# Kernel optimization log

Measured on AMD Instinct MI355X. Metric: run time of the kernel, lower is better.

## Reference

```python
import jax, jax.numpy as jnp
import numpy as np

# static config (matches init_kwargs)
B, H, W, C = 8, 64, 64, 512
HEADS, WS, SHIFT = 16, 8, 4
N = WS * WS
HIDDEN = 4 * C
HEAD_DIM = C // HEADS
SCALE = HEAD_DIM ** -0.5
EPS = 1e-3  # keras LayerNormalization default epsilon


def _rel_pos_index(ws):
    # replicates tf.meshgrid default 'xy' indexing used in the source
    coords = np.stack(np.meshgrid(np.arange(ws), np.arange(ws)))  # [2, ws, ws]
    cf = coords.reshape(2, -1)
    rel = (cf[:, :, None] - cf[:, None, :]).transpose(1, 2, 0)  # [N, N, 2]
    rel[:, :, 0] += ws - 1
    rel[:, :, 1] += ws - 1
    rel[:, :, 0] *= 2 * ws - 1
    return jnp.asarray(rel.sum(-1))  # [N, N] int


def _attn_mask(h, w, ws, shift):
    img = np.zeros((h, w), dtype=np.float32)
    cnt = 0
    for hs in (slice(0, -ws), slice(-ws, -shift), slice(-shift, None)):
        for wsl in (slice(0, -ws), slice(-ws, -shift), slice(-shift, None)):
            img[hs, wsl] = cnt
            cnt += 1
    mw = img.reshape(h // ws, ws, w // ws, ws).transpose(0, 2, 1, 3).reshape(-1, ws * ws)  # [nW, N]
    diff = mw[:, None, :] - mw[:, :, None]
    return jnp.asarray(np.where(diff != 0, -100.0, 0.0).astype(np.float32))  # [nW, N, N]


REL_IDX = _rel_pos_index(WS)
ATTN_MASK = _attn_mask(H, W, WS, SHIFT)
NW = (H // WS) * (W // WS)


def _ln(x, g, b):
    mu = jnp.mean(x, -1, keepdims=True)
    var = jnp.mean(jnp.square(x - mu), -1, keepdims=True)
    return (x - mu) * jax.lax.rsqrt(var + EPS) * g + b


def setup_inputs() -> dict:
    key = jax.random.key(0)
    ks = jax.random.split(key, 14)
    s = 0.02
    return {
        "x": jax.random.normal(ks[0], (B, H * W, C), jnp.float32),
        "norm1_g": jnp.ones((C,), jnp.float32),
        "norm1_b": jnp.zeros((C,), jnp.float32),
        "qkv_w": jax.random.normal(ks[1], (C, 3 * C), jnp.float32) * s,
        "qkv_b": jnp.zeros((3 * C,), jnp.float32),
        "rpb_table": jax.random.normal(ks[2], ((2 * WS - 1) ** 2, HEADS), jnp.float32) * s,
        "proj_w": jax.random.normal(ks[3], (C, C), jnp.float32) * s,
        "proj_b": jnp.zeros((C,), jnp.float32),
        "norm2_g": jnp.ones((C,), jnp.float32),
        "norm2_b": jnp.zeros((C,), jnp.float32),
        "fc1_w": jax.random.normal(ks[4], (C, HIDDEN), jnp.float32) * s,
        "fc1_b": jnp.zeros((HIDDEN,), jnp.float32),
        "fc2_w": jax.random.normal(ks[5], (HIDDEN, C), jnp.float32) * s,
        "fc2_b": jnp.zeros((C,), jnp.float32),
    }


def reference(x, norm1_g, norm1_b, qkv_w, qkv_b, rpb_table, proj_w, proj_b,
              norm2_g, norm2_b, fc1_w, fc1_b, fc2_w, fc2_b):
    shortcut = x
    h = _ln(x, norm1_g, norm1_b).reshape(B, H, W, C)
    # cyclic shift (SW-MSA)
    h = jnp.roll(h, (-SHIFT, -SHIFT), axis=(1, 2))
    # window partition -> (B*nW, N, C)
    h = h.reshape(B, H // WS, WS, W // WS, WS, C).transpose(0, 1, 3, 2, 4, 5)
    h = h.reshape(B * NW, N, C)
    # qkv
    qkv = (h @ qkv_w + qkv_b).reshape(B * NW, N, 3, HEADS, HEAD_DIM).transpose(2, 0, 3, 1, 4)
    q, k, v = qkv[0] * SCALE, qkv[1], qkv[2]  # each [Bw, heads, N, hd]
    attn = jnp.einsum('bhnd,bhmd->bhnm', q, k)  # [Bw, heads, N, N]
    bias = rpb_table[REL_IDX.reshape(-1)].reshape(N, N, HEADS).transpose(2, 0, 1)
    attn = attn + bias[None]
    # shifted-window mask, per source: mask add -> softmax -> softmax AGAIN (source quirk)
    attn = attn.reshape(B, NW, HEADS, N, N) + ATTN_MASK[None, :, None]
    attn = attn.reshape(B * NW, HEADS, N, N)
    attn = jax.nn.softmax(attn, axis=-1)
    attn = jax.nn.softmax(attn, axis=-1)
    o = jnp.einsum('bhnm,bhmd->bhnd', attn, v).transpose(0, 2, 1, 3).reshape(B * NW, N, C)
    o = o @ proj_w + proj_b
    # window reverse + reverse shift
    o = o.reshape(B, H // WS, W // WS, WS, WS, C).transpose(0, 1, 3, 2, 4, 5).reshape(B, H, W, C)
    o = jnp.roll(o, (SHIFT, SHIFT), axis=(1, 2)).reshape(B, H * W, C)
    x = shortcut + o
    # MLP: source applies gelu twice (Dense activation + explicit gelu)
    y = _ln(x, norm2_g, norm2_b)
    y = jax.nn.gelu(jax.nn.gelu(y @ fc1_w + fc1_b, approximate=False), approximate=False)
    y = y @ fc2_w + fc2_b
    return x + y
```

## Files before the change

kernel.cpp:

```cpp
#include <hip/hip_runtime.h>
#include <hip/hip_bf16.h>
#include <math.h>


typedef unsigned short ushort_t;
typedef __attribute__((ext_vector_type(8))) short short8;
typedef __attribute__((ext_vector_type(8))) __bf16 bf16x8;
typedef __attribute__((ext_vector_type(4))) float f32x4;

#define DEVINL __device__ __forceinline__

union frag_u { short8 s; bf16x8 b; };

DEVINL float bf2f(ushort_t u){ union {unsigned int i; float f;} c; c.i = ((unsigned)u)<<16; return c.f; }
DEVINL ushort_t f2bf(float f){ union {unsigned int i; float f;} c; c.f = f; unsigned r = c.i + 0x7fffu + ((c.i>>16)&1u); return (ushort_t)(r>>16); }

typedef const __attribute__((address_space(1))) void* gas_t;
typedef __attribute__((address_space(3))) void* las_t;
DEVINL void load_lds16(const void* g, void* l) {
  __builtin_amdgcn_global_load_lds((gas_t)g, (las_t)l, 16, 0, 0);
}

DEVINL float gelu_fast(float v){
  float z  = fabsf(v) * 0.70710678118654752f;
  float t  = __builtin_amdgcn_rcpf(fmaf(0.47047f, z, 1.0f));
  float p  = t * fmaf(t, fmaf(t, 0.7478556f, -0.0958798f), 0.3480242f);
  float e  = __expf(-z*z);
  float er = fmaf(-p, e, 1.0f);
  float hs = (v >= 0.f) ? 0.5f : -0.5f;
  return v * fmaf(hs, er, 0.5f);
}

DEVINL int win_map_row(int t){
  int bw = t >> 6, n = t & 63;
  int b  = bw >> 6, wdx = bw & 63;
  int wh = wdx >> 3, ww = wdx & 7;
  int r  = n >> 3,  c  = n & 7;
  int hh = (wh*8 + r + 4) & 63;
  int w2 = (ww*8 + c + 4) & 63;
  return (b << 12) + (hh << 6) + w2;
}

__global__ void transpose_f2b(const float* __restrict__ in, ushort_t* __restrict__ out,
                              int R, int Ccols){
  __shared__ float t[32][33];
  int bx = blockIdx.x*32, by = blockIdx.y*32;
  int x = threadIdx.x, y = threadIdx.y;
  #pragma unroll
  for (int i=0;i<32;i+=8) t[y+i][x] = in[(size_t)(by+y+i)*Ccols + bx + x];
  __syncthreads();
  #pragma unroll
  for (int i=0;i<32;i+=8) out[(size_t)(bx+y+i)*R + by + x] = f2bf(t[x][y+i]);
}

__global__ __launch_bounds__(256) void ln_kernel(const float* __restrict__ in,
    const float* __restrict__ g, const float* __restrict__ bta,
    ushort_t* __restrict__ out, int windowed){
  int tid = threadIdx.x; int l = tid & 63; int w = tid >> 6;
  int t = blockIdx.x * 4 + w;
  int src = windowed ? win_map_row(t) : t;
  const float* row = in + (size_t)src * 512;
  float4 v0 = *(const float4*)(row + l*8);
  float4 v1 = *(const float4*)(row + l*8 + 4);
  float f[8] = {v0.x,v0.y,v0.z,v0.w, v1.x,v1.y,v1.z,v1.w};
  float s=0.f, s2=0.f;
  #pragma unroll
  for (int j=0;j<8;j++){ s += f[j]; s2 += f[j]*f[j]; }
  #pragma unroll
  for (int m=1;m<64;m<<=1){ s += __shfl_xor(s,m); s2 += __shfl_xor(s2,m); }
  float mu  = s * (1.f/512.f);
  float var = s2*(1.f/512.f) - mu*mu;
  float rs  = rsqrtf(var + 1e-3f);
  float4 g0 = *(const float4*)(g + l*8),   g1 = *(const float4*)(g + l*8 + 4);
  float4 b0 = *(const float4*)(bta + l*8), b1 = *(const float4*)(bta + l*8 + 4);
  float gg[8] = {g0.x,g0.y,g0.z,g0.w, g1.x,g1.y,g1.z,g1.w};
  float bb[8] = {b0.x,b0.y,b0.z,b0.w, b1.x,b1.y,b1.z,b1.w};
  short8 o;
  #pragma unroll
  for (int j=0;j<8;j++) o[j] = (short)f2bf((f[j]-mu)*rs*gg[j] + bb[j]);
  *(short8*)(out + (size_t)t*512 + l*8) = o;
}

template<int EPI>
__global__ __launch_bounds__(256, 2) void gemm_bt(
    const ushort_t* __restrict__ A, const ushort_t* __restrict__ Bt,
    const float* __restrict__ bias, void* __restrict__ Cout_v,
    const float* __restrict__ xres, int M, int N, int K)
{
  __shared__ ushort_t lA[128*32];
  __shared__ ushort_t lB[128*32];
  int tid = threadIdx.x; int l = tid & 63; int w = tid >> 6;
  int m0 = blockIdx.x*128, n0 = blockIdx.y*128;
  int wr = (w>>1)*64, wc = (w&1)*64;
  int lr = l & 15, lk = l >> 4;

  f32x4 acc[4][4] = {};
  for (int k0 = 0; k0 < K; k0 += 32) {
    #pragma unroll
    for (int i=0;i<2;i++){
      int s   = i*256 + tid;
      int row = s >> 2;
      int cg  = ((s&3) - (row>>1)) & 3;
      ushort_t* ldst  = lA + (size_t)(i*256 + w*64)*8;
      load_lds16(A  + (size_t)(m0+row)*K + (k0 + cg*8), ldst);
      ushort_t* ldstB = lB + (size_t)(i*256 + w*64)*8;
      load_lds16(Bt + (size_t)(n0+row)*K + (k0 + cg*8), ldstB);
    }
    __syncthreads();
    bf16x8 af[4], bfr[4];
    #pragma unroll
    for (int m=0;m<4;m++){
      int row  = wr + m*16 + lr;
      int slot = row*4 + ((lk + (row>>1)) & 3);
      af[m] = *(const bf16x8*)(lA + slot*8);
    }
    #pragma unroll
    for (int n=0;n<4;n++){
      int row  = wc + n*16 + lr;
      int slot = row*4 + ((lk + (row>>1)) & 3);
      bfr[n] = *(const bf16x8*)(lB + slot*8);
    }
    #pragma unroll
    for (int m=0;m<4;m++)
      #pragma unroll
      for (int n=0;n<4;n++)
        acc[m][n] = __builtin_amdgcn_mfma_f32_16x16x32_bf16(af[m], bfr[n], acc[m][n], 0,0,0);
    __syncthreads();
  }
  #pragma unroll
  for (int m=0;m<4;m++){
    int rloc = wr + m*16 + lk*4;
    #pragma unroll
    for (int n=0;n<4;n++){
      int col = n0 + wc + n*16 + lr;
      float bz = bias[col];
      #pragma unroll
      for (int r=0;r<4;r++){
        int grow = m0 + rloc + r;
        float v = acc[m][n][r] + bz;
        if (EPI == 1) v = gelu_fast(gelu_fast(v));
        if (EPI == 0 || EPI == 1){
          ((ushort_t*)Cout_v)[(size_t)grow*N + col] = f2bf(v);
        } else if (EPI == 2){
          int row2 = win_map_row(grow);
          size_t off = (size_t)row2*512 + col;
          ((float*)Cout_v)[off] = xres[off] + v;
        } else {
          size_t off = (size_t)grow*N + col;
          ((float*)Cout_v)[off] += v;
        }
      }
    }
  }
}

#define G_STAGE(G, base, h, tt, LB) do { \
    load_lds16((G) + (base) + (size_t)((h)*128)*K    + (size_t)(tt)*64, &lds[(LB) + (h)*8192 +        w*512]); \
    load_lds16((G) + (base) + (size_t)((h)*128+64)*K + (size_t)(tt)*64, &lds[(LB) + (h)*8192 + 4096 + w*512]); \
  } while(0)

#define NOWAIT
#define VM4 asm volatile("s_waitcnt vmcnt(4)" ::: "memory")

#define PHASE(mp, STAGE_STMT, EXTRA) do { \
    bf16x8 a0 = *(const bf16x8*)&lds[ALb + aoff[2*(mp)  ][0]]; \
    bf16x8 a1 = *(const bf16x8*)&lds[ALb + aoff[2*(mp)  ][1]]; \
    bf16x8 a2 = *(const bf16x8*)&lds[ALb + aoff[2*(mp)+1][0]]; \
    bf16x8 a3 = *(const bf16x8*)&lds[ALb + aoff[2*(mp)+1][1]]; \
    STAGE_STMT; \
    EXTRA; \
    __builtin_amdgcn_s_barrier(); \
    asm volatile("s_waitcnt lgkmcnt(0)" ::: "memory"); \
    __builtin_amdgcn_sched_barrier(0); \
    __builtin_amdgcn_s_setprio(1); \
    _Pragma("unroll") \
    for (int nf=0; nf<4; nf++){ \
      acc[2*(mp)  ][nf] = __builtin_amdgcn_mfma_f32_16x16x32_bf16(a0, bfr[nf][0], acc[2*(mp)  ][nf], 0,0,0); \
      acc[2*(mp)  ][nf] = __builtin_amdgcn_mfma_f32_16x16x32_bf16(a1, bfr[nf][1], acc[2*(mp)  ][nf], 0,0,0); \
      acc[2*(mp)+1][nf] = __builtin_amdgcn_mfma_f32_16x16x32_bf16(a2, bfr[nf][0], acc[2*(mp)+1][nf], 0,0,0); \
      acc[2*(mp)+1][nf] = __builtin_amdgcn_mfma_f32_16x16x32_bf16(a3, bfr[nf][1], acc[2*(mp)+1][nf], 0,0,0); \
    } \
    __builtin_amdgcn_s_setprio(0); \
    __builtin_amdgcn_sched_barrier(0); \
    __builtin_amdgcn_s_barrier(); \
  } while(0)

template<int EPI>
__global__ __launch_bounds__(512, 2) void gemm256(
    const ushort_t* __restrict__ A, const ushort_t* __restrict__ Bt,
    const float* __restrict__ bias, void* __restrict__ Cout_v,
    const float* __restrict__ xres, int M, int N, int K)
{
  __shared__ ushort_t lds[65536];
  const int tid = threadIdx.x; const int l = tid & 63; const int w = tid >> 6;
  const int wm = w >> 2, wn = w & 3;
  const int m0 = blockIdx.x*256, n0 = blockIdx.y*256;
  const int lr = l & 15, lk = l >> 4;
  const int nt = K >> 6;

  const int r0 = tid >> 3;
  const int kc = ((tid & 7) - r0) & 7;
  const size_t aRow0 = (size_t)(m0 + r0) * K + kc * 8;
  const size_t bRow0 = (size_t)(n0 + r0) * K + kc * 8;

  int aoff[8][2], boff[4][2];
  #pragma unroll
  for (int mf=0; mf<8; mf++){
    int row = wm*128 + mf*16 + lr;
    #pragma unroll
    for (int kh=0; kh<2; kh++){ int c = kh*4 + lk; aoff[mf][kh] = (row*8 + ((c + row)&7))*8; }
  }
  #pragma unroll
  for (int nf=0; nf<4; nf++){
    int row = wn*64 + nf*16 + lr;
    #pragma unroll
    for (int kh=0; kh<2; kh++){ int c = kh*4 + lk; boff[nf][kh] = (row*8 + ((c + row)&7))*8; }
  }

  f32x4 acc[8][4] = {};

  G_STAGE(A,  aRow0, 0, 0, 0);
  G_STAGE(A,  aRow0, 1, 0, 0);
  G_STAGE(Bt, bRow0, 0, 0, 16384);
  G_STAGE(Bt, bRow0, 1, 0, 16384);
  G_STAGE(Bt, bRow0, 0, 1, 32768+16384);
  G_STAGE(Bt, bRow0, 1, 1, 32768+16384);
  VM4;
  __builtin_amdgcn_s_barrier();

  for (int t = 0; t < nt; ++t) {
    const int b   = t & 1;
    const int ALb = b*32768, BLb = ALb + 16384;
    const int ALn = (b^1)*32768;
    const int t1  = (t+1 < nt) ? t+1 : t;
    const int t2  = (t+2 < nt) ? t+2 : t;

    bf16x8 bfr[4][2];
    #pragma unroll
    for (int nf=0; nf<4; nf++){
      bfr[nf][0] = *(const bf16x8*)&lds[BLb + boff[nf][0]];
      bfr[nf][1] = *(const bf16x8*)&lds[BLb + boff[nf][1]];
    }
    PHASE(0, G_STAGE(A,  aRow0, 0, t1, ALn), NOWAIT);
    PHASE(1, G_STAGE(A,  aRow0, 1, t1, ALn), NOWAIT);
    PHASE(2, G_STAGE(Bt, bRow0, 0, t2, BLb), NOWAIT);
    PHASE(3, G_STAGE(Bt, bRow0, 1, t2, BLb), VM4);
  }

  #pragma unroll
  for (int mf=0; mf<8; mf++){
    int rbase = m0 + wm*128 + mf*16 + lk*4;
    #pragma unroll
    for (int nf=0; nf<4; nf++){
      int col = n0 + wn*64 + nf*16 + lr;
      float bz = bias[col];
      #pragma unroll
      for (int rg=0; rg<4; rg++){
        int grow = rbase + rg;
        float v = acc[mf][nf][rg] + bz;
        if (EPI == 1) v = gelu_fast(gelu_fast(v));
        if (EPI == 0 || EPI == 1){
          ((ushort_t*)Cout_v)[(size_t)grow*N + col] = f2bf(v);
        } else if (EPI == 2){
          int row2 = win_map_row(grow);
          size_t off = (size_t)row2*512 + col;
          ((float*)Cout_v)[off] = xres[off] + v;
        } else {
          size_t off = (size_t)grow*N + col;
          ((float*)Cout_v)[off] += v;
        }
      }
    }
  }
}

DEVINL int band3(int t){ return (t<56) ? 0 : ((t<60) ? 1 : 2); }

__global__ __launch_bounds__(256) void attn_kernel(const ushort_t* __restrict__ qkv,
    const float* __restrict__ rpb, ushort_t* __restrict__ o)
{
  __shared__ ushort_t sP[4][64*64];
  __shared__ ushort_t sV[4][64*32];
  int tid = threadIdx.x; int l = tid & 63; int w = tid >> 6;
  int p = blockIdx.x*4 + w;
  int bw = p >> 4, head = p & 15;
  int lr = l & 15, lk = l >> 4;
  const ushort_t* base = qkv + (size_t)bw*64*1536 + head*32;

  #pragma unroll
  for (int c=0;c<4;c++){
    int idx = c*64 + l;
    int row = idx >> 2, cc = idx & 3;
    load_lds16(base + 1024 + (size_t)row*1536 + cc*8, &sV[w][0] + c*512);
  }

  bf16x8 qf[4], kf[4];
  #pragma unroll
  for (int m=0;m<4;m++) qf[m] = *(const bf16x8*)(base +       (size_t)(m*16+lr)*1536 + lk*8);
  #pragma unroll
  for (int m=0;m<4;m++) kf[m] = *(const bf16x8*)(base + 512 + (size_t)(m*16+lr)*1536 + lk*8);

  f32x4 s[4][4] = {};
  #pragma unroll
  for (int m=0;m<4;m++)
    #pragma unroll
    for (int n=0;n<4;n++)
      s[m][n] = __builtin_amdgcn_mfma_f32_16x16x32_bf16(qf[m], kf[n], s[m][n], 0,0,0);

  int wdx = bw & 63; int wh = wdx >> 3, ww = wdx & 7;
  const float SCALE = 0.17677669529663687f;
  #pragma unroll
  for (int m=0;m<4;m++){
    #pragma unroll
    for (int r=0;r<4;r++){
      int i  = m*16 + lk*4 + r;
      int ri = band3(wh*8 + (i>>3))*3 + band3(ww*8 + (i&7));
      int ix = i & 7, iy = i >> 3;
      #pragma unroll
      for (int n=0;n<4;n++){
        int j   = n*16 + lr;
        int rj  = band3(wh*8 + (j>>3))*3 + band3(ww*8 + (j&7));
        int idx = 15*(ix - (j&7) + 7) + (iy - (j>>3) + 7);
        float bv = rpb[idx*16 + head];
        float mk = (ri == rj) ? 0.f : -100.f;
        s[m][n][r] = s[m][n][r]*SCALE + bv + mk;
      }
    }
  }

  #pragma unroll
  for (int pass=0; pass<2; pass++){
    #pragma unroll
    for (int m=0;m<4;m++){
      #pragma unroll
      for (int r=0;r<4;r++){
        float mx = fmaxf(fmaxf(s[m][0][r], s[m][1][r]), fmaxf(s[m][2][r], s[m][3][r]));
        #pragma unroll
        for (int d=1;d<16;d<<=1) mx = fmaxf(mx, __shfl_xor(mx, d));
        float sum = 0.f;
        #pragma unroll
        for (int n=0;n<4;n++){ float e = __expf(s[m][n][r]-mx); s[m][n][r]=e; sum += e; }
        #pragma unroll
        for (int d=1;d<16;d<<=1) sum += __shfl_xor(sum, d);
        float inv = 1.f/sum;
        #pragma unroll
        for (int n=0;n<4;n++) s[m][n][r] = s[m][n][r]*inv;
      }
    }
  }

  ushort_t* pl = &sP[w][0];
  #pragma unroll
  for (int m=0;m<4;m++)
    #pragma unroll
    for (int r=0;r<4;r++){
      int i = m*16 + lk*4 + r;
      #pragma unroll
      for (int n=0;n<4;n++){
        int j = n*16 + lr;
        int byte = i*128 + ((j*2) ^ ((i&7)<<4));
        pl[byte>>1] = f2bf(s[m][n][r]);
      }
    }

  asm volatile("s_waitcnt vmcnt(0)" ::: "memory");
  const ushort_t* vl = &sV[w][0];
  frag_u vf[2][2];
  #pragma unroll
  for (int kb=0;kb<2;kb++)
    #pragma unroll
    for (int nb=0;nb<2;nb++){
      #pragma unroll
      for (int j=0;j<8;j++){
        int k = kb*32 + lk*8 + j;
        vf[kb][nb].s[j] = (short)vl[k*32 + nb*16 + lr];
      }
    }

  f32x4 oacc[4][2] = {};
  #pragma unroll
  for (int m=0;m<4;m++){
    #pragma unroll
    for (int kb=0;kb<2;kb++){
      int row  = m*16 + lr;
      int byte = row*128 + ((kb*64 + lk*16) ^ ((row&7)<<4));
      bf16x8 pf = *(const bf16x8*)(pl + (byte>>1));
      #pragma unroll
      for (int nb=0;nb<2;nb++)
        oacc[m][nb] = __builtin_amdgcn_mfma_f32_16x16x32_bf16(pf, vf[kb][nb].b, oacc[m][nb], 0,0,0);
    }
  }

  ushort_t* orow = o + (size_t)bw*64*512 + head*32;
  #pragma unroll
  for (int m=0;m<4;m++)
    #pragma unroll
    for (int nb=0;nb<2;nb++)
      #pragma unroll
      for (int r=0;r<4;r++){
        int i = m*16 + lk*4 + r;
        int d = nb*16 + lr;
        orow[(size_t)i*512 + d] = f2bf(oacc[m][nb][r]);
      }
}

extern "C" void kernel_launch(void* const* d_in, const int* in_sizes, int n_in,
                              void* d_out, int out_size, void* d_ws, size_t ws_size,
                              hipStream_t stream) {
  const float* x      = (const float*)d_in[0];
  const float* n1g    = (const float*)d_in[1];
  const float* n1b    = (const float*)d_in[2];
  const float* qkv_w  = (const float*)d_in[3];
  const float* qkv_b  = (const float*)d_in[4];
  const float* rpb    = (const float*)d_in[5];
  const float* proj_w = (const float*)d_in[6];
  const float* proj_b = (const float*)d_in[7];
  const float* n2g    = (const float*)d_in[8];
  const float* n2b    = (const float*)d_in[9];
  const float* fc1_w  = (const float*)d_in[10];
  const float* fc1_b  = (const float*)d_in[11];
  const float* fc2_w  = (const float*)d_in[12];
  const float* fc2_b  = (const float*)d_in[13];
  float* out = (float*)d_out;

  ushort_t* ws = (ushort_t*)d_ws;
  size_t off = 0;
  ushort_t* wqT = ws + off; off += (size_t)1536*512;
  ushort_t* wpT = ws + off; off += (size_t)512*512;
  ushort_t* w1T = ws + off; off += (size_t)2048*512;
  ushort_t* w2T = ws + off; off += (size_t)512*2048;
  ushort_t* R1  = ws + off; off += (size_t)32768*512;
  ushort_t* R2  = ws + off; off += (size_t)32768*2048;
  if (ws_size < off*sizeof(ushort_t)) return;

  dim3 tb(32,8);
  transpose_f2b<<<dim3(48,16), tb, 0, stream>>>(qkv_w, wqT, 512, 1536);
  transpose_f2b<<<dim3(16,16), tb, 0, stream>>>(proj_w, wpT, 512, 512);
  transpose_f2b<<<dim3(64,16), tb, 0, stream>>>(fc1_w, w1T, 512, 2048);
  transpose_f2b<<<dim3(16,64), tb, 0, stream>>>(fc2_w, w2T, 2048, 512);

  ln_kernel<<<8192, 256, 0, stream>>>(x, n1g, n1b, R1, 1);
  gemm256<0><<<dim3(128, 6), 512, 0, stream>>>(R1, wqT, qkv_b, R2, nullptr, 32768, 1536, 512);
  attn_kernel<<<2048, 256, 0, stream>>>(R2, rpb, R1);
  gemm256<2><<<dim3(128, 2), 512, 0, stream>>>(R1, wpT, proj_b, out, x, 32768, 512, 512);
  ln_kernel<<<8192, 256, 0, stream>>>(out, n2g, n2b, R1, 0);
  gemm_bt<1><<<dim3(256, 16), 256, 0, stream>>>(R1, w1T, fc1_b, R2, nullptr, 32768, 2048, 512);
  gemm256<3><<<dim3(128, 2), 512, 0, stream>>>(R2, w2T, fc2_b, out, nullptr, 32768, 512, 2048);
}
```

Before: 445.9 us.

## Stage GEMM epilogues through LDS for vectorized stores and merge weight transposes

The GEMM epilogues now write each wave's 16-row accumulator tile into shared memory, then read it back row-contiguous so every lane issues 16-byte vector stores (bf16 outputs) or float4 loads and stores (residual outputs), replacing scattered 2- and 4-byte per-element accesses. The four weight-transpose launches are merged into one kernel that picks its matrix from the block index, saving launch overhead. In exchange the epilogue adds LDS round-trips plus a full vmcnt wait and barrier before reusing the pipeline buffers. Staging correctness depends on the per-wave LDS regions not overlapping live data.

```diff
diff --git a/kernel.cpp b/kernel.cpp
--- a/kernel.cpp
+++ b/kernel.cpp
@@ -41,10 +41,17 @@
   return (b << 12) + (hh << 6) + w2;
 }
 
-__global__ void transpose_f2b(const float* __restrict__ in, ushort_t* __restrict__ out,
-                              int R, int Ccols){
+__global__ void transpose_all(const float* __restrict__ qkv_w, const float* __restrict__ proj_w,
+                              const float* __restrict__ fc1_w, const float* __restrict__ fc2_w,
+                              ushort_t* __restrict__ wqT, ushort_t* __restrict__ wpT,
+                              ushort_t* __restrict__ w1T, ushort_t* __restrict__ w2T){
   __shared__ float t[32][33];
-  int bx = blockIdx.x*32, by = blockIdx.y*32;
+  int bid = blockIdx.x;
+  const float* in; ushort_t* out; int R, Ccols, bx, by;
+  if (bid < 768)      { in=qkv_w;  out=wqT; R=512;  Ccols=1536; bx=(bid%48)*32;        by=(bid/48)*32; }
+  else if (bid < 1024){ int b=bid-768;  in=proj_w; out=wpT; R=512;  Ccols=512;  bx=(b%16)*32; by=(b/16)*32; }
+  else if (bid < 2048){ int b=bid-1024; in=fc1_w;  out=w1T; R=512;  Ccols=2048; bx=(b%64)*32; by=(b/64)*32; }
+  else                { int b=bid-2048; in=fc2_w;  out=w2T; R=2048; Ccols=512;  bx=(b%16)*32; by=(b/16)*32; }
   int x = threadIdx.x, y = threadIdx.y;
   #pragma unroll
   for (int i=0;i<32;i+=8) t[y+i][x] = in[(size_t)(by+y+i)*Ccols + bx + x];
@@ -87,8 +94,9 @@
     const float* __restrict__ bias, void* __restrict__ Cout_v,
     const float* __restrict__ xres, int M, int N, int K)
 {
-  __shared__ ushort_t lA[128*32];
-  __shared__ ushort_t lB[128*32];
+  __shared__ ushort_t lAB[2*128*32];
+  ushort_t* lA = lAB;
+  ushort_t* lB = lAB + 128*32;
   int tid = threadIdx.x; int l = tid & 63; int w = tid >> 6;
   int m0 = blockIdx.x*128, n0 = blockIdx.y*128;
   int wr = (w>>1)*64, wc = (w&1)*64;
@@ -127,27 +135,49 @@
         acc[m][n] = __builtin_amdgcn_mfma_f32_16x16x32_bf16(af[m], bfr[n], acc[m][n], 0,0,0);
     __syncthreads();
   }
-  #pragma unroll
-  for (int m=0;m<4;m++){
-    int rloc = wr + m*16 + lk*4;
-    #pragma unroll
-    for (int n=0;n<4;n++){
-      int col = n0 + wc + n*16 + lr;
-      float bz = bias[col];
-      #pragma unroll
-      for (int r=0;r<4;r++){
-        int grow = m0 + rloc + r;
-        float v = acc[m][n][r] + bz;
-        if (EPI == 1) v = gelu_fast(gelu_fast(v));
-        if (EPI == 0 || EPI == 1){
-          ((ushort_t*)Cout_v)[(size_t)grow*N + col] = f2bf(v);
-        } else if (EPI == 2){
-          int row2 = win_map_row(grow);
-          size_t off = (size_t)row2*512 + col;
-          ((float*)Cout_v)[off] = xres[off] + v;
-        } else {
-          size_t off = (size_t)grow*N + col;
-          ((float*)Cout_v)[off] += v;
+
+  if (EPI == 0 || EPI == 1){
+    ushort_t* tw = lAB + w*1152;
+    int row = l >> 2, cc = l & 3;
+    #pragma unroll
+    for (int m=0;m<4;m++){
+      #pragma unroll
+      for (int n=0;n<4;n++){
+        float bz = bias[n0 + wc + n*16 + lr];
+        #pragma unroll
+        for (int r=0;r<4;r++){
+          float v = acc[m][n][r] + bz;
+          if (EPI == 1) v = gelu_fast(gelu_fast(v));
+          tw[(lk*4+r)*72 + n*16 + lr] = f2bf(v);
+        }
+      }
+      short8 p0 = *(const short8*)(tw + row*72 + cc*16);
+      short8 p1 = *(const short8*)(tw + row*72 + cc*16 + 8);
+      int grow = m0 + wr + m*16 + row;
+      int col  = n0 + wc + cc*16;
+      *(short8*)&((ushort_t*)Cout_v)[(size_t)grow*N + col]     = p0;
+      *(short8*)&((ushort_t*)Cout_v)[(size_t)grow*N + col + 8] = p1;
+    }
+  } else {
+    #pragma unroll
+    for (int m=0;m<4;m++){
+      int rloc = wr + m*16 + lk*4;
+      #pragma unroll
+      for (int n=0;n<4;n++){
+        int col = n0 + wc + n*16 + lr;
+        float bz = bias[col];
+        #pragma unroll
+        for (int r=0;r<4;r++){
+          int grow = m0 + rloc + r;
+          float v = acc[m][n][r] + bz;
+          if (EPI == 2){
+            int row2 = win_map_row(grow);
+            size_t off = (size_t)row2*512 + col;
+            ((float*)Cout_v)[off] = xres[off] + v;
+          } else {
+            size_t off = (size_t)grow*N + col;
+            ((float*)Cout_v)[off] += v;
+          }
         }
       }
     }
@@ -247,29 +277,74 @@
     PHASE(3, G_STAGE(Bt, bRow0, 1, t2, BLb), VM4);
   }
 
-  #pragma unroll
-  for (int mf=0; mf<8; mf++){
-    int rbase = m0 + wm*128 + mf*16 + lk*4;
-    #pragma unroll
-    for (int nf=0; nf<4; nf++){
-      int col = n0 + wn*64 + nf*16 + lr;
-      float bz = bias[col];
-      #pragma unroll
-      for (int rg=0; rg<4; rg++){
-        int grow = rbase + rg;
-        float v = acc[mf][nf][rg] + bz;
-        if (EPI == 1) v = gelu_fast(gelu_fast(v));
-        if (EPI == 0 || EPI == 1){
-          ((ushort_t*)Cout_v)[(size_t)grow*N + col] = f2bf(v);
-        } else if (EPI == 2){
-          int row2 = win_map_row(grow);
-          size_t off = (size_t)row2*512 + col;
-          ((float*)Cout_v)[off] = xres[off] + v;
-        } else {
-          size_t off = (size_t)grow*N + col;
-          ((float*)Cout_v)[off] += v;
-        }
-      }
+  asm volatile("s_waitcnt vmcnt(0)" ::: "memory");
+  __builtin_amdgcn_s_barrier();
+
+  int erow = l >> 2, ecc = l & 3;
+  if (EPI == 0){
+    ushort_t* tw = lds + w*1152;
+    #pragma unroll
+    for (int mf=0; mf<8; mf++){
+      #pragma unroll
+      for (int nf=0; nf<4; nf++){
+        float bz = bias[n0 + wn*64 + nf*16 + lr];
+        #pragma unroll
+        for (int rg=0; rg<4; rg++)
+          tw[(lk*4+rg)*72 + nf*16 + lr] = f2bf(acc[mf][nf][rg] + bz);
+      }
+      short8 p0 = *(const short8*)(tw + erow*72 + ecc*16);
+      short8 p1 = *(const short8*)(tw + erow*72 + ecc*16 + 8);
+      int grow = m0 + wm*128 + mf*16 + erow;
+      int col  = n0 + wn*64 + ecc*16;
+      *(short8*)&((ushort_t*)Cout_v)[(size_t)grow*N + col]     = p0;
+      *(short8*)&((ushort_t*)Cout_v)[(size_t)grow*N + col + 8] = p1;
+    }
+  } else {
+    float* twf = (float*)lds + w*1152;
+    #pragma unroll
+    for (int mf=0; mf<8; mf++){
+      #pragma unroll
+      for (int nf=0; nf<4; nf++){
+        float bz = bias[n0 + wn*64 + nf*16 + lr];
+        #pragma unroll
+        for (int rg=0; rg<4; rg++)
+          twf[(lk*4+rg)*72 + nf*16 + lr] = acc[mf][nf][rg] + bz;
+      }
+      int grow = m0 + wm*128 + mf*16 + erow;
+      int col  = n0 + wn*64 + ecc*16;
+      float4 q0 = *(const float4*)(twf + erow*72 + ecc*16);
+      float4 q1 = *(const float4*)(twf + erow*72 + ecc*16 + 4);
+      float4 q2 = *(const float4*)(twf + erow*72 + ecc*16 + 8);
+      float4 q3 = *(const float4*)(twf + erow*72 + ecc*16 + 12);
+      size_t off;
+      if (EPI == 2){
+        int row2 = win_map_row(grow);
+        off = (size_t)row2*512 + col;
+        float4 x0 = *(const float4*)(xres + off);
+        float4 x1 = *(const float4*)(xres + off + 4);
+        float4 x2 = *(const float4*)(xres + off + 8);
+        float4 x3 = *(const float4*)(xres + off + 12);
+        q0 = make_float4(q0.x+x0.x, q0.y+x0.y, q0.z+x0.z, q0.w+x0.w);
+        q1 = make_float4(q1.x+x1.x, q1.y+x1.y, q1.z+x1.z, q1.w+x1.w);
+        q2 = make_float4(q2.x+x2.x, q2.y+x2.y, q2.z+x2.z, q2.w+x2.w);
+        q3 = make_float4(q3.x+x3.x, q3.y+x3.y, q3.z+x3.z, q3.w+x3.w);
+      } else {
+        off = (size_t)grow*N + col;
+        float* o = (float*)Cout_v;
+        float4 x0 = *(const float4*)(o + off);
+        float4 x1 = *(const float4*)(o + off + 4);
+        float4 x2 = *(const float4*)(o + off + 8);
+        float4 x3 = *(const float4*)(o + off + 12);
+        q0 = make_float4(q0.x+x0.x, q0.y+x0.y, q0.z+x0.z, q0.w+x0.w);
+        q1 = make_float4(q1.x+x1.x, q1.y+x1.y, q1.z+x1.z, q1.w+x1.w);
+        q2 = make_float4(q2.x+x2.x, q2.y+x2.y, q2.z+x2.z, q2.w+x2.w);
+        q3 = make_float4(q3.x+x3.x, q3.y+x3.y, q3.z+x3.z, q3.w+x3.w);
+      }
+      float* o = (float*)Cout_v;
+      *(float4*)(o + off)      = q0;
+      *(float4*)(o + off + 4)  = q1;
+      *(float4*)(o + off + 8)  = q2;
+      *(float4*)(o + off + 12) = q3;
     }
   }
 }
@@ -433,11 +508,7 @@
   ushort_t* R2  = ws + off; off += (size_t)32768*2048;
   if (ws_size < off*sizeof(ushort_t)) return;
 
-  dim3 tb(32,8);
-  transpose_f2b<<<dim3(48,16), tb, 0, stream>>>(qkv_w, wqT, 512, 1536);
-  transpose_f2b<<<dim3(16,16), tb, 0, stream>>>(proj_w, wpT, 512, 512);
-  transpose_f2b<<<dim3(64,16), tb, 0, stream>>>(fc1_w, w1T, 512, 2048);
-  transpose_f2b<<<dim3(16,64), tb, 0, stream>>>(fc2_w, w2T, 2048, 512);
+  transpose_all<<<3072, dim3(32,8), 0, stream>>>(qkv_w, proj_w, fc1_w, fc2_w, wqT, wpT, w1T, w2T);
 
   ln_kernel<<<8192, 256, 0, stream>>>(x, n1g, n1b, R1, 1);
   gemm256<0><<<dim3(128, 6), 512, 0, stream>>>(R1, wqT, qkv_b, R2, nullptr, 32768, 1536, 512);
```

Result: faster. 423.7 us (-5.0%).
